# Performance work log

Hardware: AMD Instinct MI355X
Metric: run time of the kernel (lower is better)

## Reference

```python
import jax, jax.numpy as jnp
import numpy as np

D_MODEL = 2048
H_Q = 32
H_KV = 8
D_HEAD = D_MODEL // H_Q  # 64
Q_PER_KV = H_Q // H_KV   # 4
B, L = 2, 2048


def setup_inputs() -> dict:
    key = jax.random.key(0)
    kx, kq, kk, kv, ko = jax.random.split(key, 5)
    s = 0.02
    return {
        "x": jax.random.normal(kx, (B, L, D_MODEL), dtype=jnp.float32),
        "Wq": jax.random.normal(kq, (D_MODEL, D_MODEL), dtype=jnp.float32) * s,
        "Wk": jax.random.normal(kk, (D_MODEL, D_HEAD * H_KV), dtype=jnp.float32) * s,
        "Wv": jax.random.normal(kv, (D_MODEL, D_HEAD * H_KV), dtype=jnp.float32) * s,
        "Wo": jax.random.normal(ko, (D_MODEL, D_MODEL), dtype=jnp.float32) * s,
    }


def reference(x, Wq, Wk, Wv, Wo):
    Bb, Ll, _ = x.shape
    # Projections (nn.Linear with bias=False -> x @ W; weights stored as (in, out))
    Q = (x @ Wq).reshape(Bb, Ll, H_Q, D_HEAD)          # (B, L, Hq, d)
    K = (x @ Wk).reshape(Bb, Ll, H_KV, D_HEAD)         # (B, L, Hkv, d)
    V = (x @ Wv).reshape(Bb, Ll, H_KV, D_HEAD)
    # Group query heads: (B, Hkv, q_per_kv, L, d)
    Q = Q.transpose(0, 2, 1, 3).reshape(Bb, H_KV, Q_PER_KV, Ll, D_HEAD)
    K = K.transpose(0, 2, 1, 3)                        # (B, Hkv, L, d)
    V = V.transpose(0, 2, 1, 3)
    scale = 1.0 / jnp.sqrt(jnp.asarray(D_HEAD, dtype=x.dtype))
    # scores: (B, Hkv, q_per_kv, L, L)
    scores = jnp.einsum('bhgqd,bhkd->bhgqk', Q, K) * scale
    attn = jax.nn.softmax(scores, axis=-1)
    out = jnp.einsum('bhgqk,bhkd->bhgqd', attn, V)     # (B, Hkv, g, L, d)
    out = out.reshape(Bb, H_Q, Ll, D_HEAD).transpose(0, 2, 1, 3).reshape(Bb, Ll, D_MODEL)
    return out @ Wo
```

## Files before the change

kernel.cpp:

```cpp
#include <hip/hip_runtime.h>
#include <hip/hip_bf16.h>
#include <cstdint>
#include <cmath>

#define D_MODEL 2048
#define HQ 32
#define HKV 8
#define DH 64
#define NB 2
#define LSEQ 2048
#define MROWS (NB*LSEQ)
#define KVB 64

typedef __attribute__((ext_vector_type(8))) short short8;
typedef __attribute__((ext_vector_type(4))) float f32x4;
typedef __attribute__((ext_vector_type(4))) unsigned short ushort4v;
typedef __attribute__((ext_vector_type(4))) unsigned int uint4v;
typedef unsigned short ushort;

#if __has_builtin(__builtin_amdgcn_exp2f)
#define EXP2(x) __builtin_amdgcn_exp2f(x)
#else
#define EXP2(x) exp2f(x)
#endif

__device__ __forceinline__ ushort f2bf(float f) {
    unsigned u = __float_as_uint(f);
    u += 0x7fffu + ((u >> 16) & 1u);
    return (ushort)(u >> 16);
}

__device__ __forceinline__ unsigned cvtpk_sp(float a, float b) {
    unsigned r;
    asm("s_nop 1\n\tv_cvt_pk_bf16_f32 %0, %1, %2" : "=v"(r) : "v"(a), "v"(b));
    return r;
}

__device__ __forceinline__ void gload_lds16(const ushort* gsrc, ushort* ldst) {
    __builtin_amdgcn_global_load_lds((const __attribute__((address_space(1))) void*)gsrc,
                                     (__attribute__((address_space(3))) void*)ldst, 16, 0, 0);
}

__global__ __launch_bounds__(256)
void cvt_bf16_k(const float* __restrict__ in, ushort* __restrict__ out, int n4) {
    int i = blockIdx.x * blockDim.x + threadIdx.x;
    if (i < n4) {
        float4 v = *(const float4*)(in + (size_t)i * 4);
        ushort4v o = {f2bf(v.x), f2bf(v.y), f2bf(v.z), f2bf(v.w)};
        *(ushort4v*)(out + (size_t)i * 4) = o;
    }
}

__global__ __launch_bounds__(256)
void transpose_all(const float* __restrict__ Wq, const float* __restrict__ Wk,
                   const float* __restrict__ Wv, const float* __restrict__ Wo,
                   ushort* __restrict__ dst) {
    __shared__ float t[32][33];
    const int tid = threadIdx.x;
    const int n0 = blockIdx.x * 32, k0 = blockIdx.y * 32;
    const float* W; int Nd, nl;
    if (n0 < 2048)      { W = Wq; Nd = 2048; nl = n0; }
    else if (n0 < 2560) { W = Wk; Nd = 512;  nl = n0 - 2048; }
    else if (n0 < 3072) { W = Wv; Nd = 512;  nl = n0 - 2560; }
    else                { W = Wo; Nd = 2048; nl = n0 - 3072; }
    const int r = tid >> 3, c4 = (tid & 7) << 2;
    float4 v = *(const float4*)(W + (size_t)(k0 + r) * Nd + nl + c4);
    t[r][c4 + 0] = v.x; t[r][c4 + 1] = v.y; t[r][c4 + 2] = v.z; t[r][c4 + 3] = v.w;
    __syncthreads();
    const int n = tid >> 3, kc = (tid & 7) << 2;
    ushort4v o = {f2bf(t[kc + 0][n]), f2bf(t[kc + 1][n]), f2bf(t[kc + 2][n]), f2bf(t[kc + 3][n])};
    *(ushort4v*)(dst + (size_t)(n0 + n) * 2048 + k0 + kc) = o;
}

template<int BM, int MODE>
__global__ __launch_bounds__(256, 2)
void gemm_bf16(const ushort* __restrict__ A, const ushort* __restrict__ Bt,
               void* __restrict__ Cv, int M, int N, int K, float scale)
{
    constexpr int BN = 128;
    constexpr int FM = BM / 32;
    constexpr int ISSA = BM / 64;
    __shared__ __align__(16) ushort smem[2 * (BM + BN) * 32];
    ushort* As = smem;
    ushort* Bs = smem + 2 * BM * 32;

    const int tid = threadIdx.x;
    const int w = tid >> 6;
    const int wr = w >> 1, wc = w & 1;
    const int g = (tid & 63) >> 4, r16 = tid & 15;
    const int bm = blockIdx.y * BM, bn = blockIdx.x * BN;
    const int srow = tid >> 2, sphys = tid & 3;

    f32x4 acc[FM][4];
#pragma unroll
    for (int i = 0; i < FM; ++i)
#pragma unroll
        for (int j = 0; j < 4; ++j) acc[i][j] = {0.f, 0.f, 0.f, 0.f};

    auto stage = [&](int buf, int k0) {
#pragma unroll
        for (int i = 0; i < ISSA; ++i) {
            int row = i * 64 + srow;
            int slog = sphys ^ ((row >> 1) & 3);
            gload_lds16(A + (size_t)(bm + row) * K + k0 + slog * 8,
                        As + buf * BM * 32 + (i * 64 + w * 16) * 32);
        }
#pragma unroll
        for (int i = 0; i < 2; ++i) {
            int row = i * 64 + srow;
            int slog = sphys ^ ((row >> 1) & 3);
            gload_lds16(Bt + (size_t)(bn + row) * K + k0 + slog * 8,
                        Bs + buf * 128 * 32 + (i * 64 + w * 16) * 32);
        }
    };

    const int NTk = K >> 5;
    stage(0, 0);
    __syncthreads();
    int buf = 0;
    for (int kt = 0; kt < NTk; ++kt) {
        if (kt + 1 < NTk) stage(buf ^ 1, (kt + 1) << 5);
        const ushort* Ab = As + buf * BM * 32;
        const ushort* Bb = Bs + buf * 128 * 32;
        short8 af[FM], bfv[4];
#pragma unroll
        for (int mi = 0; mi < FM; ++mi) {
            int row = wr * (BM / 2) + mi * 16 + r16;
            int p = g ^ ((row >> 1) & 3);
            af[mi] = *(const short8*)(Ab + row * 32 + p * 8);
        }
#pragma unroll
        for (int ni = 0; ni < 4; ++ni) {
            int row = wc * 64 + ni * 16 + r16;
            int p = g ^ ((row >> 1) & 3);
            bfv[ni] = *(const short8*)(Bb + row * 32 + p * 8);
        }
#pragma unroll
        for (int mi = 0; mi < FM; ++mi)
#pragma unroll
            for (int ni = 0; ni < 4; ++ni)
                acc[mi][ni] = __builtin_amdgcn_mfma_f32_16x16x32_bf16(af[mi], bfv[ni], acc[mi][ni], 0, 0, 0);
        __syncthreads();
        buf ^= 1;
    }

    float* C = (float*)Cv;
#pragma unroll
    for (int mi = 0; mi < FM; ++mi)
#pragma unroll
        for (int ni = 0; ni < 4; ++ni)
#pragma unroll
            for (int r = 0; r < 4; ++r) {
                int row = bm + wr * (BM / 2) + mi * 16 + g * 4 + r;
                int col = bn + wc * 64 + ni * 16 + r16;
                C[(size_t)row * N + col] = acc[mi][ni][r] * scale;
            }
}

__global__ __launch_bounds__(256, 2)
void gemm_qkv(const ushort* __restrict__ A, const ushort* __restrict__ Bt,
              ushort* __restrict__ Qd, ushort* __restrict__ Kd, ushort* __restrict__ Vd,
              float qscale)
{
    constexpr int K = 2048;
    __shared__ __align__(16) ushort smem[2 * 256 * 32];

    const int tid = threadIdx.x;
    const int l = tid & 63;
    const int w = tid >> 6;
    const int wr = w >> 1, wc = w & 1;
    const int g = l >> 4, r16 = l & 15;
    const int bm = blockIdx.y * 128, bn = blockIdx.x * 128;
    const int srow = tid >> 2, sphys = tid & 3;

    ushort* As = smem;
    ushort* Bs = smem + 2 * 128 * 32;

    f32x4 acc[4][4];
#pragma unroll
    for (int i = 0; i < 4; ++i)
#pragma unroll
        for (int j = 0; j < 4; ++j) acc[i][j] = {0.f, 0.f, 0.f, 0.f};

    auto stage = [&](int buf, int k0) {
#pragma unroll
        for (int i = 0; i < 2; ++i) {
            int row = i * 64 + srow;
            int slog = sphys ^ ((row >> 1) & 3);
            gload_lds16(A + (size_t)(bm + row) * K + k0 + slog * 8,
                        As + buf * 128 * 32 + (i * 64 + w * 16) * 32);
            gload_lds16(Bt + (size_t)(bn + row) * K + k0 + slog * 8,
                        Bs + buf * 128 * 32 + (i * 64 + w * 16) * 32);
        }
    };

    stage(0, 0);
    __syncthreads();
    int buf = 0;
    for (int kt = 0; kt < K / 32; ++kt) {
        if (kt + 1 < K / 32) stage(buf ^ 1, (kt + 1) << 5);
        const ushort* Ab = As + buf * 128 * 32;
        const ushort* Bb = Bs + buf * 128 * 32;
        short8 af[4], bfv[4];
#pragma unroll
        for (int mi = 0; mi < 4; ++mi) {
            int row = wr * 64 + mi * 16 + r16;
            int p = g ^ ((row >> 1) & 3);
            af[mi] = *(const short8*)(Ab + row * 32 + p * 8);
        }
#pragma unroll
        for (int ni = 0; ni < 4; ++ni) {
            int row = wc * 64 + ni * 16 + r16;
            int p = g ^ ((row >> 1) & 3);
            bfv[ni] = *(const short8*)(Bb + row * 32 + p * 8);
        }
#pragma unroll
        for (int mi = 0; mi < 4; ++mi)
#pragma unroll
            for (int ni = 0; ni < 4; ++ni)
                acc[mi][ni] = __builtin_amdgcn_mfma_f32_16x16x32_bf16(af[mi], bfv[ni], acc[mi][ni], 0, 0, 0);
        __syncthreads();
        buf ^= 1;
    }

    const int colbase = bn + wc * 64;
    const int rowbase = bm + wr * 64;
    const int b = rowbase >> 11;
    const int l0 = rowbase & (LSEQ - 1);
    ushort* Ls = smem + w * 64 * 64;
    __syncthreads();

    if (colbase < 2560) {
        const float sc = (colbase < 2048) ? qscale : 1.f;
#pragma unroll
        for (int mi = 0; mi < 4; ++mi)
#pragma unroll
            for (int ni = 0; ni < 4; ++ni)
#pragma unroll
                for (int r = 0; r < 4; ++r)
                    Ls[(mi * 16 + g * 4 + r) * 64 + ni * 16 + r16] = f2bf(acc[mi][ni][r] * sc);
        __syncthreads();
        ushort* dst;
        if (colbase < 2048)
            dst = Qd + (((size_t)(b * 32 + (colbase >> 6))) * LSEQ + l0) * 64;
        else
            dst = Kd + (((size_t)(b * 8 + ((colbase - 2048) >> 6))) * LSEQ + l0) * 64;
#pragma unroll
        for (int c = 0; c < 8; ++c) {
            int idx = c * 64 + l;
            *(short8*)(dst + idx * 8) = *(const short8*)(Ls + idx * 8);
        }
    } else {
#pragma unroll
        for (int mi = 0; mi < 4; ++mi)
#pragma unroll
            for (int ni = 0; ni < 4; ++ni) {
                ushort4v pk = {f2bf(acc[mi][ni][0]), f2bf(acc[mi][ni][1]),
                               f2bf(acc[mi][ni][2]), f2bf(acc[mi][ni][3])};
                *(ushort4v*)(&Ls[(((mi >> 1) * 64 + ni * 16 + r16) * 4 + g) * 8 + (mi & 1) * 4]) = pk;
            }
        __syncthreads();
        const int h = (colbase - 2560) >> 6;
        ushort* dst = Vd + (((size_t)(b * 8 + h)) * 64 + (l0 >> 5)) * 2048;
#pragma unroll
        for (int c = 0; c < 8; ++c) {
            int idx = c * 64 + l;
            *(short8*)(dst + (size_t)idx * 8) = *(const short8*)(Ls + idx * 8);
        }
    }
}

__global__ __launch_bounds__(256, 2)
void attn_bf16(const ushort* __restrict__ Qb, const ushort* __restrict__ Kb,
               const ushort* __restrict__ Vtb, ushort* __restrict__ Ob)
{
    __shared__ __align__(16) ushort Ks[2][KVB * 64];
    __shared__ __align__(16) ushort Vs[2][KVB * 64];

    const int tid = threadIdx.x;
    const int l = tid & 63, w = tid >> 6;
    const int g = l >> 4, r16 = l & 15;
    const int bh = blockIdx.y, b = bh >> 5, hq = bh & 31, hk = hq >> 2;
    const int q0 = blockIdx.x * 256 + w * 64;

    const ushort* Qh = Qb + (size_t)bh * LSEQ * 64;
    const ushort* Kh = Kb + (size_t)(b * HKV + hk) * LSEQ * 64;
    const ushort* Vh = Vtb + (size_t)(b * HKV + hk) * 64 * LSEQ;

    short8 qf[4][2];
#pragma unroll
    for (int qb = 0; qb < 4; ++qb)
#pragma unroll
        for (int dh = 0; dh < 2; ++dh)
            qf[qb][dh] = *(const short8*)(Qh + (size_t)(q0 + qb * 16 + r16) * 64 + dh * 32 + g * 8);

    short8 ones;
#pragma unroll
    for (int j = 0; j < 8; ++j) ones[j] = (short)0x3F80;

    f32x4 acco[4][4];
#pragma unroll
    for (int i = 0; i < 4; ++i)
#pragma unroll
        for (int j = 0; j < 4; ++j) acco[i][j] = {0.f, 0.f, 0.f, 0.f};
    f32x4 accl[4] = {{0,0,0,0},{0,0,0,0},{0,0,0,0},{0,0,0,0}};

    const int sr = tid >> 3, sp = tid & 7;

    auto stage = [&](ushort* kdst, ushort* vdst, int k0) {
        const int slog = sp ^ (sr & 7);
#pragma unroll
        for (int i = 0; i < 2; ++i)
            gload_lds16(Kh + (size_t)(k0 + i * 32 + sr) * 64 + slog * 8,
                        kdst + i * 2048 + w * 512);
#pragma unroll
        for (int i = 0; i < 2; ++i)
            gload_lds16(Vh + (size_t)k0 * 64 + i * 2048 + (size_t)tid * 8,
                        vdst + i * 2048 + w * 512);
    };

    auto body = [&](const ushort* Kc, const ushort* Vc, ushort* Kn, ushort* Vn, int t) {
        if (t + 1 < LSEQ / KVB) stage(Kn, Vn, (t + 1) * KVB);

        uint4v pw[2][4];
#pragma unroll
        for (int kb = 0; kb < 4; ++kb) {
            const int row = kb * 16 + r16, c = r16 & 7;
            short8 kf0 = *(const short8*)(Kc + row * 64 + ((g) ^ c) * 8);
            short8 kf1 = *(const short8*)(Kc + row * 64 + ((4 + g) ^ c) * 8);
#pragma unroll
            for (int qb = 0; qb < 4; ++qb) {
                f32x4 z = {0.f, 0.f, 0.f, 0.f};
                z = __builtin_amdgcn_mfma_f32_16x16x32_bf16(kf0, qf[qb][0], z, 0, 0, 0);
                f32x4 sq = __builtin_amdgcn_mfma_f32_16x16x32_bf16(kf1, qf[qb][1], z, 0, 0, 0);
                float p0 = EXP2(sq[0]), p1 = EXP2(sq[1]);
                float p2 = EXP2(sq[2]), p3 = EXP2(sq[3]);
                pw[kb >> 1][qb][(kb & 1) * 2 + 0] = cvtpk_sp(p0, p1);
                pw[kb >> 1][qb][(kb & 1) * 2 + 1] = cvtpk_sp(p2, p3);
            }
        }

        short8 vf[4][2];
#pragma unroll
        for (int db = 0; db < 4; ++db)
#pragma unroll
            for (int s = 0; s < 2; ++s)
                vf[db][s] = *(const short8*)(Vc + ((s * 64 + db * 16 + r16) * 4 + g) * 8);

#pragma unroll
        for (int db = 0; db < 4; ++db)
#pragma unroll
            for (int qb = 0; qb < 4; ++qb) {
                acco[db][qb] = __builtin_amdgcn_mfma_f32_16x16x32_bf16(
                    vf[db][0], *(short8*)&pw[0][qb], acco[db][qb], 0, 0, 0);
                acco[db][qb] = __builtin_amdgcn_mfma_f32_16x16x32_bf16(
                    vf[db][1], *(short8*)&pw[1][qb], acco[db][qb], 0, 0, 0);
            }
#pragma unroll
        for (int qb = 0; qb < 4; ++qb) {
            accl[qb] = __builtin_amdgcn_mfma_f32_16x16x32_bf16(
                ones, *(short8*)&pw[0][qb], accl[qb], 0, 0, 0);
            accl[qb] = __builtin_amdgcn_mfma_f32_16x16x32_bf16(
                ones, *(short8*)&pw[1][qb], accl[qb], 0, 0, 0);
        }

        __syncthreads();
    };

    stage(Ks[0], Vs[0], 0);
    __syncthreads();
    for (int kt = 0; kt < LSEQ / KVB; kt += 2) {
        body(Ks[0], Vs[0], Ks[1], Vs[1], kt);
        body(Ks[1], Vs[1], Ks[0], Vs[0], kt + 1);
    }

    float inv[4] = {1.f / accl[0][0], 1.f / accl[1][0], 1.f / accl[2][0], 1.f / accl[3][0]};
#pragma unroll
    for (int qb = 0; qb < 4; ++qb)
#pragma unroll
        for (int db = 0; db < 4; ++db) {
            int lseq = q0 + qb * 16 + r16;
            ushort4v o = {f2bf(acco[db][qb][0] * inv[qb]), f2bf(acco[db][qb][1] * inv[qb]),
                          f2bf(acco[db][qb][2] * inv[qb]), f2bf(acco[db][qb][3] * inv[qb])};
            *(ushort4v*)(Ob + ((size_t)b * LSEQ + lseq) * D_MODEL + hq * 64 + db * 16 + g * 4) = o;
        }
}

extern "C" void kernel_launch(void* const* d_in, const int* in_sizes, int n_in,
                              void* d_out, int out_size, void* d_ws, size_t ws_size,
                              hipStream_t stream)
{
    const float* x  = (const float*)d_in[0];
    const float* Wq = (const float*)d_in[1];
    const float* Wk = (const float*)d_in[2];
    const float* Wv = (const float*)d_in[3];
    const float* Wo = (const float*)d_in[4];

    ushort* xb  = (ushort*)d_ws;
    ushort* Ob  = xb;
    ushort* Wf  = xb  + (size_t)MROWS * D_MODEL;
    ushort* Wot = Wf  + (size_t)3072 * D_MODEL;
    ushort* Kbf = Wot + (size_t)D_MODEL * D_MODEL;
    ushort* Vtb = Kbf + (size_t)NB * HKV * LSEQ * DH;
    ushort* Qbf = (ushort*)d_out;

    dim3 blk(256);
    cvt_bf16_k<<<dim3((MROWS * D_MODEL / 4 + 255) / 256), blk, 0, stream>>>(x, xb, MROWS * D_MODEL / 4);
    transpose_all<<<dim3(5120 / 32, D_MODEL / 32), blk, 0, stream>>>(Wq, Wk, Wv, Wo, Wf);

    gemm_qkv<<<dim3(3072 / 128, MROWS / 128), blk, 0, stream>>>(
        xb, Wf, Qbf, Kbf, Vtb, 0.125f * 1.44269504f);

    attn_bf16<<<dim3(LSEQ / 256, NB * HQ), blk, 0, stream>>>(Qbf, Kbf, Vtb, Ob);

    gemm_bf16<128, 0><<<dim3(D_MODEL / 128, MROWS / 128), blk, 0, stream>>>(
        Ob, Wot, d_out, MROWS, D_MODEL, D_MODEL, 1.f);
}
```

Baseline: 191.9 us.

## Fuse x fp32-to-bf16 conversion into QKV GEMM and halve attention query tile

The separate conversion kernel for x is removed. gemm_qkv now loads fp32 x tiles into registers, converts them to bf16 and writes them into swizzled LDS after the MFMA work, which avoids an extra round trip of the activation through global memory and one kernel launch. The cost is more global read bytes per tile, because fp32 x is re-read by each of the 24 column blocks, plus register-staged rather than async LDS loads for A. Separately, the attention kernel now gives each wave 32 query rows instead of 64, doubling the grid to improve occupancy and load balance at the cost of more K/V tile reloads.

```diff
diff --git a/kernel.cpp b/kernel.cpp
--- a/kernel.cpp
+++ b/kernel.cpp
@@ -39,16 +39,6 @@
 __device__ __forceinline__ void gload_lds16(const ushort* gsrc, ushort* ldst) {
     __builtin_amdgcn_global_load_lds((const __attribute__((address_space(1))) void*)gsrc,
                                      (__attribute__((address_space(3))) void*)ldst, 16, 0, 0);
-}
-
-__global__ __launch_bounds__(256)
-void cvt_bf16_k(const float* __restrict__ in, ushort* __restrict__ out, int n4) {
-    int i = blockIdx.x * blockDim.x + threadIdx.x;
-    if (i < n4) {
-        float4 v = *(const float4*)(in + (size_t)i * 4);
-        ushort4v o = {f2bf(v.x), f2bf(v.y), f2bf(v.z), f2bf(v.w)};
-        *(ushort4v*)(out + (size_t)i * 4) = o;
-    }
 }
 
 __global__ __launch_bounds__(256)
@@ -158,7 +148,7 @@
 }
 
 __global__ __launch_bounds__(256, 2)
-void gemm_qkv(const ushort* __restrict__ A, const ushort* __restrict__ Bt,
+void gemm_qkv(const float* __restrict__ A, const ushort* __restrict__ Bt,
               ushort* __restrict__ Qd, ushort* __restrict__ Kd, ushort* __restrict__ Vd,
               float qscale)
 {
@@ -172,6 +162,7 @@
     const int g = l >> 4, r16 = l & 15;
     const int bm = blockIdx.y * 128, bn = blockIdx.x * 128;
     const int srow = tid >> 2, sphys = tid & 3;
+    const int ar = tid >> 3, ac = tid & 7;
 
     ushort* As = smem;
     ushort* Bs = smem + 2 * 128 * 32;
@@ -182,23 +173,40 @@
 #pragma unroll
         for (int j = 0; j < 4; ++j) acc[i][j] = {0.f, 0.f, 0.f, 0.f};
 
-    auto stage = [&](int buf, int k0) {
+    auto loadA = [&](float4* regs, int k0) {
+#pragma unroll
+        for (int i = 0; i < 4; ++i)
+            regs[i] = *(const float4*)(A + (size_t)(bm + i * 32 + ar) * K + k0 + ac * 4);
+    };
+    auto writeA = [&](int buf, const float4* regs) {
+        const int slog = ac >> 1, half = ac & 1;
+#pragma unroll
+        for (int i = 0; i < 4; ++i) {
+            int row = i * 32 + ar;
+            int p = slog ^ ((row >> 1) & 3);
+            ushort4v pk = {f2bf(regs[i].x), f2bf(regs[i].y), f2bf(regs[i].z), f2bf(regs[i].w)};
+            *(ushort4v*)(As + buf * 128 * 32 + row * 32 + p * 8 + half * 4) = pk;
+        }
+    };
+    auto stageB = [&](int buf, int k0) {
 #pragma unroll
         for (int i = 0; i < 2; ++i) {
             int row = i * 64 + srow;
             int slog = sphys ^ ((row >> 1) & 3);
-            gload_lds16(A + (size_t)(bm + row) * K + k0 + slog * 8,
-                        As + buf * 128 * 32 + (i * 64 + w * 16) * 32);
             gload_lds16(Bt + (size_t)(bn + row) * K + k0 + slog * 8,
                         Bs + buf * 128 * 32 + (i * 64 + w * 16) * 32);
         }
     };
 
-    stage(0, 0);
+    float4 aregs[4];
+    loadA(aregs, 0);
+    stageB(0, 0);
+    writeA(0, aregs);
     __syncthreads();
     int buf = 0;
     for (int kt = 0; kt < K / 32; ++kt) {
-        if (kt + 1 < K / 32) stage(buf ^ 1, (kt + 1) << 5);
+        const bool pre = (kt + 1 < K / 32);
+        if (pre) { loadA(aregs, (kt + 1) << 5); stageB(buf ^ 1, (kt + 1) << 5); }
         const ushort* Ab = As + buf * 128 * 32;
         const ushort* Bb = Bs + buf * 128 * 32;
         short8 af[4], bfv[4];
@@ -219,6 +227,7 @@
 #pragma unroll
             for (int ni = 0; ni < 4; ++ni)
                 acc[mi][ni] = __builtin_amdgcn_mfma_f32_16x16x32_bf16(af[mi], bfv[ni], acc[mi][ni], 0, 0, 0);
+        if (pre) writeA(buf ^ 1, aregs);
         __syncthreads();
         buf ^= 1;
     }
@@ -281,15 +290,15 @@
     const int l = tid & 63, w = tid >> 6;
     const int g = l >> 4, r16 = l & 15;
     const int bh = blockIdx.y, b = bh >> 5, hq = bh & 31, hk = hq >> 2;
-    const int q0 = blockIdx.x * 256 + w * 64;
+    const int q0 = blockIdx.x * 128 + w * 32;
 
     const ushort* Qh = Qb + (size_t)bh * LSEQ * 64;
     const ushort* Kh = Kb + (size_t)(b * HKV + hk) * LSEQ * 64;
     const ushort* Vh = Vtb + (size_t)(b * HKV + hk) * 64 * LSEQ;
 
-    short8 qf[4][2];
-#pragma unroll
-    for (int qb = 0; qb < 4; ++qb)
+    short8 qf[2][2];
+#pragma unroll
+    for (int qb = 0; qb < 2; ++qb)
 #pragma unroll
         for (int dh = 0; dh < 2; ++dh)
             qf[qb][dh] = *(const short8*)(Qh + (size_t)(q0 + qb * 16 + r16) * 64 + dh * 32 + g * 8);
@@ -298,12 +307,12 @@
 #pragma unroll
     for (int j = 0; j < 8; ++j) ones[j] = (short)0x3F80;
 
-    f32x4 acco[4][4];
+    f32x4 acco[4][2];
 #pragma unroll
     for (int i = 0; i < 4; ++i)
 #pragma unroll
-        for (int j = 0; j < 4; ++j) acco[i][j] = {0.f, 0.f, 0.f, 0.f};
-    f32x4 accl[4] = {{0,0,0,0},{0,0,0,0},{0,0,0,0},{0,0,0,0}};
+        for (int j = 0; j < 2; ++j) acco[i][j] = {0.f, 0.f, 0.f, 0.f};
+    f32x4 accl[2] = {{0,0,0,0},{0,0,0,0}};
 
     const int sr = tid >> 3, sp = tid & 7;
 
@@ -322,14 +331,14 @@
     auto body = [&](const ushort* Kc, const ushort* Vc, ushort* Kn, ushort* Vn, int t) {
         if (t + 1 < LSEQ / KVB) stage(Kn, Vn, (t + 1) * KVB);
 
-        uint4v pw[2][4];
+        uint4v pw[2][2];
 #pragma unroll
         for (int kb = 0; kb < 4; ++kb) {
             const int row = kb * 16 + r16, c = r16 & 7;
             short8 kf0 = *(const short8*)(Kc + row * 64 + ((g) ^ c) * 8);
             short8 kf1 = *(const short8*)(Kc + row * 64 + ((4 + g) ^ c) * 8);
 #pragma unroll
-            for (int qb = 0; qb < 4; ++qb) {
+            for (int qb = 0; qb < 2; ++qb) {
                 f32x4 z = {0.f, 0.f, 0.f, 0.f};
                 z = __builtin_amdgcn_mfma_f32_16x16x32_bf16(kf0, qf[qb][0], z, 0, 0, 0);
                 f32x4 sq = __builtin_amdgcn_mfma_f32_16x16x32_bf16(kf1, qf[qb][1], z, 0, 0, 0);
@@ -350,14 +359,14 @@
 #pragma unroll
         for (int db = 0; db < 4; ++db)
 #pragma unroll
-            for (int qb = 0; qb < 4; ++qb) {
+            for (int qb = 0; qb < 2; ++qb) {
                 acco[db][qb] = __builtin_amdgcn_mfma_f32_16x16x32_bf16(
                     vf[db][0], *(short8*)&pw[0][qb], acco[db][qb], 0, 0, 0);
                 acco[db][qb] = __builtin_amdgcn_mfma_f32_16x16x32_bf16(
                     vf[db][1], *(short8*)&pw[1][qb], acco[db][qb], 0, 0, 0);
             }
 #pragma unroll
-        for (int qb = 0; qb < 4; ++qb) {
+        for (int qb = 0; qb < 2; ++qb) {
             accl[qb] = __builtin_amdgcn_mfma_f32_16x16x32_bf16(
                 ones, *(short8*)&pw[0][qb], accl[qb], 0, 0, 0);
             accl[qb] = __builtin_amdgcn_mfma_f32_16x16x32_bf16(
@@ -374,9 +383,9 @@
         body(Ks[1], Vs[1], Ks[0], Vs[0], kt + 1);
     }
 
-    float inv[4] = {1.f / accl[0][0], 1.f / accl[1][0], 1.f / accl[2][0], 1.f / accl[3][0]};
-#pragma unroll
-    for (int qb = 0; qb < 4; ++qb)
+    float inv[2] = {1.f / accl[0][0], 1.f / accl[1][0]};
+#pragma unroll
+    for (int qb = 0; qb < 2; ++qb)
 #pragma unroll
         for (int db = 0; db < 4; ++db) {
             int lseq = q0 + qb * 16 + r16;
@@ -396,22 +405,20 @@
     const float* Wv = (const float*)d_in[3];
     const float* Wo = (const float*)d_in[4];
 
-    ushort* xb  = (ushort*)d_ws;
-    ushort* Ob  = xb;
-    ushort* Wf  = xb  + (size_t)MROWS * D_MODEL;
+    ushort* Ob  = (ushort*)d_ws;
+    ushort* Wf  = Ob  + (size_t)MROWS * D_MODEL;
     ushort* Wot = Wf  + (size_t)3072 * D_MODEL;
     ushort* Kbf = Wot + (size_t)D_MODEL * D_MODEL;
     ushort* Vtb = Kbf + (size_t)NB * HKV * LSEQ * DH;
     ushort* Qbf = (ushort*)d_out;
 
     dim3 blk(256);
-    cvt_bf16_k<<<dim3((MROWS * D_MODEL / 4 + 255) / 256), blk, 0, stream>>>(x, xb, MROWS * D_MODEL / 4);
     transpose_all<<<dim3(5120 / 32, D_MODEL / 32), blk, 0, stream>>>(Wq, Wk, Wv, Wo, Wf);
 
     gemm_qkv<<<dim3(3072 / 128, MROWS / 128), blk, 0, stream>>>(
-        xb, Wf, Qbf, Kbf, Vtb, 0.125f * 1.44269504f);
-
-    attn_bf16<<<dim3(LSEQ / 256, NB * HQ), blk, 0, stream>>>(Qbf, Kbf, Vtb, Ob);
+        x, Wf, Qbf, Kbf, Vtb, 0.125f * 1.44269504f);
+
+    attn_bf16<<<dim3(LSEQ / 128, NB * HQ), blk, 0, stream>>>(Qbf, Kbf, Vtb, Ob);
 
     gemm_bf16<128, 0><<<dim3(D_MODEL / 128, MROWS / 128), blk, 0, stream>>>(
         Ob, Wot, d_out, MROWS, D_MODEL, D_MODEL, 1.f);
```

Measured after the change: 197.4 us. +2.9%, slower.
